# Kernel tuning notes

Hardware: AMD Instinct MI355X
Metric: run time of the kernel (lower is better)

The kernel has to match this reference:

```python
import jax, jax.numpy as jnp
import numpy as np

WD, WH, WW = 1, 7, 7
N = WD * WH * WW  # 49 tokens per window
LN_EPS = 1e-5


def _make_rel_coords_table():
    rd = np.arange(-(WD - 1), WD, dtype=np.float32)
    rh = np.arange(-(WH - 1), WH, dtype=np.float32)
    rw = np.arange(-(WW - 1), WW, dtype=np.float32)
    g = np.stack(np.meshgrid(rd, rh, rw, indexing='ij'), axis=-1)  # (2wd-1,2wh-1,2ww-1,3)
    eps = 1e-6
    g = g / (np.array([WD, WH, WW], np.float32) - (1.0 - eps))
    g = g * 8.0
    g = np.sign(g) * np.log2(np.abs(g) + 1.0) / np.log2(8.0)
    return g[None].astype(np.float32)  # (1,2wd-1,2wh-1,2ww-1,3)


def _make_rel_pos_index():
    coords = np.stack(np.meshgrid(np.arange(WD), np.arange(WH), np.arange(WW), indexing='ij'))
    cf = coords.reshape(3, -1)  # (3,N)
    rel = cf[:, :, None] - cf[:, None, :]  # (3,N,N)
    rel = rel.transpose(1, 2, 0).astype(np.int64)
    rel[..., 0] += WD - 1
    rel[..., 1] += WH - 1
    rel[..., 2] += WW - 1
    rel[..., 0] *= (2 * WH - 1) * (2 * WW - 1)
    rel[..., 1] *= 2 * WW - 1
    return rel.sum(-1).astype(np.int32)  # (N,N)


def setup_inputs() -> dict:
    key = jax.random.key(0)
    ks = jax.random.split(key, 8)
    B, D, H, W, C = 4, 8, 56, 56, 256
    nh, hid = 8, 4 * C

    def init_w(k, shape, fan_in):
        return (jax.random.normal(k, shape, jnp.float32) / np.sqrt(fan_in)).astype(jnp.float32)

    inp = {
        'x': jax.random.normal(ks[0], (B, D, H, W, C), jnp.float32),
        'qkv_w': init_w(ks[1], (3 * C, C), C),
        'q_bias': jnp.zeros((C,), jnp.float32),
        'v_bias': jnp.zeros((C,), jnp.float32),
        'logit_scale': jnp.full((nh, 1, 1), np.log(10.0), jnp.float32),
        'cpb_w1': init_w(ks[2], (512, 3), 3),
        'cpb_b1': jnp.zeros((512,), jnp.float32),
        'cpb_w2': init_w(ks[3], (nh, 512), 512),
        'proj_w': init_w(ks[4], (C, C), C),
        'proj_b': jnp.zeros((C,), jnp.float32),
        'norm1_g': jnp.ones((C,), jnp.float32),
        'norm1_b': jnp.zeros((C,), jnp.float32),
        'fc1_w': init_w(ks[5], (hid, C), C),
        'fc1_b': jnp.zeros((hid,), jnp.float32),
        'fc2_w': init_w(ks[6], (C, hid), hid),
        'fc2_b': jnp.zeros((C,), jnp.float32),
        'norm2_g': jnp.ones((C,), jnp.float32),
        'norm2_b': jnp.zeros((C,), jnp.float32),
        'rel_coords_table': jnp.asarray(_make_rel_coords_table()),
        'rel_pos_index': jnp.asarray(_make_rel_pos_index()),
    }
    return inp


def _layernorm(x, g, b):
    mu = jnp.mean(x, axis=-1, keepdims=True)
    var = jnp.mean(jnp.square(x - mu), axis=-1, keepdims=True)
    return (x - mu) * jax.lax.rsqrt(var + LN_EPS) * g + b


def _l2norm(x):
    # F.normalize(dim=-1): x / max(||x||, 1e-12)
    n = jnp.sqrt(jnp.sum(jnp.square(x), axis=-1, keepdims=True))
    return x / jnp.maximum(n, 1e-12)


def _forward(x, qkv_w, q_bias, v_bias, logit_scale, cpb_w1, cpb_b1, cpb_w2,
             proj_w, proj_b, norm1_g, norm1_b, fc1_w, fc1_b, fc2_w, fc2_b,
             norm2_g, norm2_b, rel_coords_table, rel_pos_index):
    B, D, H, W, C = x.shape
    nh = logit_scale.shape[0]
    hd = C // nh

    # ---- window partition: (B,D,H,W,C) -> (B_, N, C)
    xw = x.reshape(B, D // WD, WD, H // WH, WH, W // WW, WW, C)
    xw = xw.transpose(0, 1, 3, 5, 2, 4, 6, 7).reshape(-1, N, C)
    Bw = xw.shape[0]

    # ---- qkv with (q_bias, 0, v_bias)
    qkv_bias = jnp.concatenate([q_bias, jnp.zeros_like(q_bias), v_bias])
    qkv = xw @ qkv_w.T + qkv_bias  # (Bw,N,3C)
    qkv = qkv.reshape(Bw, N, 3, nh, hd).transpose(2, 0, 3, 1, 4)
    q, k, v = qkv[0], qkv[1], qkv[2]  # (Bw,nh,N,hd)

    # ---- cosine attention with clamped learned logit scale
    attn = jnp.einsum('bhnd,bhmd->bhnm', _l2norm(q), _l2norm(k))
    scale = jnp.exp(jnp.minimum(logit_scale, jnp.float32(np.log(100.0))))  # (nh,1,1)
    attn = attn * scale

    # ---- CPB-MLP relative position bias
    t = rel_coords_table.reshape(-1, 3)
    hcpb = jax.nn.relu(t @ cpb_w1.T + cpb_b1)
    table = hcpb @ cpb_w2.T  # (T, nh)
    rpb = table[rel_pos_index.reshape(-1)].reshape(N, N, nh).transpose(2, 0, 1)
    rpb = 16.0 * jax.nn.sigmoid(rpb)
    attn = attn + rpb[None]

    attn = jax.nn.softmax(attn, axis=-1)
    out = jnp.einsum('bhnm,bhmd->bhnd', attn, v)
    out = out.transpose(0, 2, 1, 3).reshape(Bw, N, C)
    out = out @ proj_w.T + proj_b

    # ---- window reverse
    xr = out.reshape(B, D // WD, H // WH, W // WW, WD, WH, WW, C)
    xr = xr.transpose(0, 1, 4, 2, 5, 3, 6, 7).reshape(B, D, H, W, C)

    # ---- Swin-v2 post-norm residuals
    x = x + _layernorm(xr, norm1_g, norm1_b)
    h = jax.nn.gelu(x @ fc1_w.T + fc1_b, approximate=False)
    y = h @ fc2_w.T + fc2_b
    x = x + _layernorm(y, norm2_g, norm2_b)
    return x


def reference(x, qkv_w, q_bias, v_bias, logit_scale, cpb_w1, cpb_b1, cpb_w2,
              proj_w, proj_b, norm1_g, norm1_b, fc1_w, fc1_b, fc2_w, fc2_b,
              norm2_g, norm2_b, rel_coords_table, rel_pos_index):
    return _forward(x, qkv_w, q_bias, v_bias, logit_scale, cpb_w1, cpb_b1, cpb_w2,
                    proj_w, proj_b, norm1_g, norm1_b, fc1_w, fc1_b, fc2_w, fc2_b,
                    norm2_g, norm2_b, rel_coords_table, rel_pos_index)
```

## Files before the change

### kernel.cpp

```cpp
#include <hip/hip_runtime.h>
#include <hip/hip_bf16.h>

typedef __attribute__((ext_vector_type(8))) short short8_t;
typedef __attribute__((ext_vector_type(4))) float f32x4;

__device__ __forceinline__ float bf2f(unsigned short u) {
    return __uint_as_float(((unsigned)u) << 16);
}
__device__ __forceinline__ unsigned short f2bf(float f) {
    __hip_bfloat16 h = __float2bfloat16(f);
    return *reinterpret_cast<unsigned short*>(&h);
}

__device__ __forceinline__ float fast_gelu(float v) {
    float ax = fabsf(v) * 0.70710678118f;
    float t  = __builtin_amdgcn_rcpf(1.f + 0.3275911f * ax);
    float poly = t * (0.254829592f + t * (-0.284496736f + t * (1.421413741f
               + t * (-1.453152027f + t * 1.061405429f))));
    float e  = __expf(-ax * ax);
    float er = 1.f - poly * e;
    float s  = (v >= 0.f) ? er : -er;
    return 0.5f * v * (1.f + s);
}

__device__ __forceinline__ void async16(const unsigned short* g, unsigned short* l) {
    __builtin_amdgcn_global_load_lds(
        (const __attribute__((address_space(1))) unsigned int*)g,
        (__attribute__((address_space(3))) unsigned int*)l,
        16, 0, 0);
}

__device__ __forceinline__ int win_row_to_token(int r) {
    int wb = r / 49, n = r - wb * 49;
    int wq = wb & 7, hb = (wb >> 3) & 7, d = (wb >> 6) & 7, b = wb >> 9;
    int hh = n / 7, ww2 = n - hh * 7;
    return ((b * 8 + d) * 56 + hb * 7 + hh) * 56 + wq * 7 + ww2;
}

__global__ __launch_bounds__(256) void conv_kernel(
    const float* __restrict__ src, unsigned short* __restrict__ dst, int n4)
{
    int stride = gridDim.x * 256;
    for (int i = blockIdx.x * 256 + threadIdx.x; i < n4; i += stride) {
        float4 v = *reinterpret_cast<const float4*>(&src[(size_t)i * 4]);
        short4 o;
        o.x = (short)f2bf(v.x); o.y = (short)f2bf(v.y);
        o.z = (short)f2bf(v.z); o.w = (short)f2bf(v.w);
        *reinterpret_cast<short4*>(&dst[(size_t)i * 4]) = o;
    }
}

__global__ __launch_bounds__(256) void conv4_kernel(
    const float* __restrict__ s0, unsigned short* __restrict__ d0, int n0,
    const float* __restrict__ s1, unsigned short* __restrict__ d1, int n1,
    const float* __restrict__ s2, unsigned short* __restrict__ d2, int n2,
    const float* __restrict__ s3, unsigned short* __restrict__ d3, int n3)
{
    int stride = gridDim.x * 256;
    int total = n0 + n1 + n2 + n3;
    for (int i = blockIdx.x * 256 + threadIdx.x; i < total; i += stride) {
        const float* s; unsigned short* d; int j = i;
        if (j < n0) { s = s0; d = d0; }
        else if ((j -= n0) < n1) { s = s1; d = d1; }
        else if ((j -= n1) < n2) { s = s2; d = d2; }
        else { j -= n2; s = s3; d = d3; }
        float4 v = *reinterpret_cast<const float4*>(&s[(size_t)j * 4]);
        short4 o;
        o.x = (short)f2bf(v.x); o.y = (short)f2bf(v.y);
        o.z = (short)f2bf(v.z); o.w = (short)f2bf(v.w);
        *reinterpret_cast<short4*>(&d[(size_t)j * 4]) = o;
    }
}

__global__ __launch_bounds__(256) void prep_table_kernel(
    const float* __restrict__ w1, const float* __restrict__ b1,
    const float* __restrict__ w2, const float* __restrict__ tabin,
    float* __restrict__ tableg)
{
    const int i = blockIdx.x;
    const int t = threadIdx.x;
    const float c0 = tabin[i * 3], c1 = tabin[i * 3 + 1], c2 = tabin[i * 3 + 2];
    float part[8] = {0.f, 0.f, 0.f, 0.f, 0.f, 0.f, 0.f, 0.f};
    for (int j = t; j < 512; j += 256) {
        float hv = fmaxf(c0 * w1[j * 3] + c1 * w1[j * 3 + 1] + c2 * w1[j * 3 + 2] + b1[j], 0.f);
        #pragma unroll
        for (int h = 0; h < 8; ++h) part[h] += hv * w2[h * 512 + j];
    }
    #pragma unroll
    for (int h = 0; h < 8; ++h) {
        float v = part[h];
        v += __shfl_xor(v, 1);  v += __shfl_xor(v, 2);  v += __shfl_xor(v, 4);
        v += __shfl_xor(v, 8);  v += __shfl_xor(v, 16); v += __shfl_xor(v, 32);
        part[h] = v;
    }
    __shared__ float red[4][8];
    const int wv = t >> 6, lane = t & 63;
    if (lane == 0) {
        #pragma unroll
        for (int h = 0; h < 8; ++h) red[wv][h] = part[h];
    }
    __syncthreads();
    if (t < 8) tableg[i * 8 + t] = red[0][t] + red[1][t] + red[2][t] + red[3][t];
}

__global__ __launch_bounds__(256) void prep_expand_kernel(
    const float* __restrict__ logit_scale,
    const float* __restrict__ qb, const float* __restrict__ vb,
    const int* __restrict__ rpi, const float* __restrict__ tableg,
    float* __restrict__ scales, float* __restrict__ rpbf,
    float* __restrict__ qkvb)
{
    const int stride = gridDim.x * 256;
    const int gt = blockIdx.x * 256 + threadIdx.x;
    if (gt < 8) scales[gt] = expf(fminf(logit_scale[gt], 4.6051702f));
    for (int i = gt; i < 768; i += stride) {
        float o;
        if (i < 256) o = qb[i];
        else if (i < 512) o = 0.f;
        else o = vb[i - 512];
        qkvb[i] = o;
    }
    for (int e = gt; e < 32768; e += stride) {
        int h = e >> 12, rem = e & 4095;
        int mi = rem >> 10, ji = (rem >> 8) & 3;
        int r16 = (rem >> 4) & 15, g4 = (rem >> 2) & 3, r = rem & 3;
        int i = mi * 16 + g4 * 4 + r, j = ji * 16 + r16;
        float val = 0.f;
        if (i < 49 && j < 49) {
            float xv = tableg[rpi[i * 49 + j] * 8 + h];
            val = 16.f / (1.f + expf(-xv));
        }
        rpbf[e] = val;
    }
}

template<int ACT, int SCATTER>
__global__ __launch_bounds__(256) void gemm_kernel(
    const unsigned short* __restrict__ A, const unsigned short* __restrict__ W,
    const float* __restrict__ bias, unsigned short* __restrict__ C,
    int M, int N, int K, int ntn)
{
    __shared__ unsigned short smem[16384];
    const int tid = threadIdx.x;
    const int lane = tid & 63, wv = tid >> 6;
    const int wr = wv >> 1, wc = wv & 1;
    const int nwg = gridDim.x;
    const int virt = (blockIdx.x & 7) * (nwg >> 3) + (blockIdx.x >> 3);
    const int bn = virt % ntn, bm = virt / ntn;
    const size_t arow0 = (size_t)bm * 128;
    const size_t brow0 = (size_t)bn * 128;
    const int r16 = lane & 15, g4 = lane >> 4;
    const int srow_l = lane >> 2;
    const int sgran  = (lane & 3) ^ ((srow_l >> 1) & 3);
    f32x4 acc[4][4] = {};

    auto STAGE = [&](int buf, int kt) {
        unsigned short* As = smem + buf * 4096;
        unsigned short* Bs = smem + 8192 + buf * 4096;
        #pragma unroll
        for (int i = 0; i < 2; ++i) {
            int row0 = wv * 32 + i * 16;
            async16(&A[(arow0 + row0 + srow_l) * (size_t)K + kt + sgran * 8], &As[row0 * 32]);
            async16(&W[(brow0 + row0 + srow_l) * (size_t)K + kt + sgran * 8], &Bs[row0 * 32]);
        }
    };
    auto COMPUTE = [&](int buf) {
        unsigned short* As = smem + buf * 4096;
        unsigned short* Bs = smem + 8192 + buf * 4096;
        short8_t af[4], bfr[4];
        const int gsw = g4 ^ ((r16 >> 1) & 3);
        #pragma unroll
        for (int m = 0; m < 4; ++m) {
            int row = wr * 64 + m * 16 + r16;
            af[m] = *reinterpret_cast<const short8_t*>(&As[row * 32 + gsw * 8]);
        }
        #pragma unroll
        for (int n = 0; n < 4; ++n) {
            int row = wc * 64 + n * 16 + r16;
            bfr[n] = *reinterpret_cast<const short8_t*>(&Bs[row * 32 + gsw * 8]);
        }
        #pragma unroll
        for (int m = 0; m < 4; ++m)
            #pragma unroll
            for (int n = 0; n < 4; ++n)
                acc[m][n] = __builtin_amdgcn_mfma_f32_16x16x32_bf16(af[m], bfr[n], acc[m][n], 0, 0, 0);
    };

    const int nk = K >> 5;
    STAGE(0, 0);
    STAGE(1, 32);
    int cur = 0;
    for (int ks = 0; ks < nk - 1; ++ks) {
        asm volatile("s_waitcnt vmcnt(4)" ::: "memory");
        __builtin_amdgcn_sched_barrier(0);
        asm volatile("s_barrier" ::: "memory");
        COMPUTE(cur);
        __builtin_amdgcn_sched_barrier(0);
        asm volatile("s_barrier" ::: "memory");
        if (ks + 2 < nk) STAGE(cur, (ks + 2) << 5);
        cur ^= 1;
    }
    asm volatile("s_waitcnt vmcnt(0)" ::: "memory");
    __builtin_amdgcn_sched_barrier(0);
    asm volatile("s_barrier" ::: "memory");
    COMPUTE(cur);
    __builtin_amdgcn_sched_barrier(0);
    asm volatile("s_barrier" ::: "memory");

    unsigned short* Cs = smem + wv * 2432;
    const int rbase = g4 * 4;
    const int srow = lane >> 3, scol = (lane & 7) * 8;
    const int gcol0 = bn * 128 + wc * 64;
    #pragma unroll
    for (int p = 0; p < 2; ++p) {
        #pragma unroll
        for (int n = 0; n < 4; ++n) {
            float bv = bias[bn * 128 + wc * 64 + n * 16 + r16];
            #pragma unroll
            for (int m2 = 0; m2 < 2; ++m2) {
                int m = p * 2 + m2;
                #pragma unroll
                for (int r = 0; r < 4; ++r) {
                    float v = acc[m][n][r] + bv;
                    if (ACT == 1) v = fast_gelu(v);
                    Cs[(m2 * 16 + rbase + r) * 76 + n * 16 + r16] = f2bf(v);
                }
            }
        }
        #pragma unroll
        for (int rr = 0; rr < 4; ++rr) {
            int lr = rr * 8 + srow;
            int grow = bm * 128 + wr * 64 + p * 32 + lr;
            size_t orow = SCATTER ? (size_t)win_row_to_token(grow) : (size_t)grow;
            short8_t vv = *reinterpret_cast<const short8_t*>(&Cs[lr * 76 + scol]);
            *reinterpret_cast<short8_t*>(&C[orow * (size_t)N + gcol0 + scol]) = vv;
        }
    }
}

template<int SCATTER, int OUT_F32>
__global__ __launch_bounds__(512) void gemm_ln_kernel(
    const unsigned short* __restrict__ A, const unsigned short* __restrict__ W,
    const float* __restrict__ bias, const unsigned short* __restrict__ resid,
    const float* __restrict__ gamma, const float* __restrict__ beta,
    void* __restrict__ Cv, int M, int K)
{
    __shared__ unsigned short smem[24576];
    const int tid = threadIdx.x;
    const int lane = tid & 63, wv = tid >> 6;
    const int wr = wv >> 2, wc = wv & 3;
    const int nwg = gridDim.x;
    const int bm = (blockIdx.x & 7) * (nwg >> 3) + (blockIdx.x >> 3);
    const size_t arow0 = (size_t)bm * 128;
    const int r16 = lane & 15, g4 = lane >> 4;
    const int srow_l = lane >> 2;
    const int sgran = (lane & 3) ^ ((srow_l >> 1) & 3);
    f32x4 acc[4][4] = {};

    auto STAGE = [&](int buf, int kt) {
        unsigned short* As = smem + buf * 4096;
        unsigned short* Bs = smem + 8192 + buf * 8192;
        async16(&A[(arow0 + wv * 16 + srow_l) * (size_t)K + kt + sgran * 8],
                &As[(wv * 16) * 32]);
        #pragma unroll
        for (int i = 0; i < 2; ++i) {
            int row0 = wv * 32 + i * 16;
            async16(&W[(size_t)(row0 + srow_l) * K + kt + sgran * 8], &Bs[row0 * 32]);
        }
    };
    auto COMPUTE = [&](int buf) {
        unsigned short* As = smem + buf * 4096;
        unsigned short* Bs = smem + 8192 + buf * 8192;
        short8_t af[4], bfr[4];
        const int gsw = g4 ^ ((r16 >> 1) & 3);
        #pragma unroll
        for (int m = 0; m < 4; ++m) {
            int row = wr * 64 + m * 16 + r16;
            af[m] = *reinterpret_cast<const short8_t*>(&As[row * 32 + gsw * 8]);
        }
        #pragma unroll
        for (int n = 0; n < 4; ++n) {
            int row = wc * 64 + n * 16 + r16;
            bfr[n] = *reinterpret_cast<const short8_t*>(&Bs[row * 32 + gsw * 8]);
        }
        #pragma unroll
        for (int m = 0; m < 4; ++m)
            #pragma unroll
            for (int n = 0; n < 4; ++n)
                acc[m][n] = __builtin_amdgcn_mfma_f32_16x16x32_bf16(af[m], bfr[n], acc[m][n], 0, 0, 0);
    };

    const int nk = K >> 5;
    STAGE(0, 0);
    STAGE(1, 32);
    int cur = 0;
    for (int ks = 0; ks < nk - 1; ++ks) {
        asm volatile("s_waitcnt vmcnt(3)" ::: "memory");
        __builtin_amdgcn_sched_barrier(0);
        asm volatile("s_barrier" ::: "memory");
        COMPUTE(cur);
        __builtin_amdgcn_sched_barrier(0);
        asm volatile("s_barrier" ::: "memory");
        if (ks + 2 < nk) STAGE(cur, (ks + 2) << 5);
        cur ^= 1;
    }
    asm volatile("s_waitcnt vmcnt(0)" ::: "memory");
    __builtin_amdgcn_sched_barrier(0);
    asm volatile("s_barrier" ::: "memory");
    COMPUTE(cur);
    __builtin_amdgcn_sched_barrier(0);
    asm volatile("s_barrier" ::: "memory");

    float bv[4];
    #pragma unroll
    for (int n = 0; n < 4; ++n) bv[n] = bias[wc * 64 + n * 16 + r16];
    float* psum  = reinterpret_cast<float*>(smem + 19456);
    float* psq   = psum + 512;
    float* stats = psq + 512;
    #pragma unroll
    for (int m = 0; m < 4; ++m) {
        #pragma unroll
        for (int r = 0; r < 4; ++r) {
            float s = 0.f, s2 = 0.f;
            #pragma unroll
            for (int n = 0; n < 4; ++n) {
                float v = acc[m][n][r] + bv[n];
                s += v; s2 += v * v;
            }
            s  += __shfl_xor(s, 1);  s  += __shfl_xor(s, 2);
            s  += __shfl_xor(s, 4);  s  += __shfl_xor(s, 8);
            s2 += __shfl_xor(s2, 1); s2 += __shfl_xor(s2, 2);
            s2 += __shfl_xor(s2, 4); s2 += __shfl_xor(s2, 8);
            if (r16 == 0) {
                int row = wr * 64 + m * 16 + g4 * 4 + r;
                psum[row * 4 + wc] = s;
                psq[row * 4 + wc]  = s2;
            }
        }
    }
    __syncthreads();
    if (tid < 128) {
        f32x4 a = *reinterpret_cast<const f32x4*>(&psum[tid * 4]);
        f32x4 b = *reinterpret_cast<const f32x4*>(&psq[tid * 4]);
        float mu  = (a[0] + a[1] + a[2] + a[3]) * 0.00390625f;
        float ex2 = (b[0] + b[1] + b[2] + b[3]) * 0.00390625f;
        stats[tid * 2]     = mu;
        stats[tid * 2 + 1] = rsqrtf(ex2 - mu * mu + 1e-5f);
    }
    __syncthreads();

    unsigned short* Cs = smem + wv * 2432;
    const int rbase = g4 * 4;
    const int srow = lane >> 3, scol = (lane & 7) * 8;
    const int gcol0 = wc * 64;
    f32x4 gm0 = *reinterpret_cast<const f32x4*>(&gamma[gcol0 + scol]);
    f32x4 gm1 = *reinterpret_cast<const f32x4*>(&gamma[gcol0 + scol + 4]);
    f32x4 bt0 = *reinterpret_cast<const f32x4*>(&beta[gcol0 + scol]);
    f32x4 bt1 = *reinterpret_cast<const f32x4*>(&beta[gcol0 + scol + 4]);
    #pragma unroll
    for (int p = 0; p < 2; ++p) {
        #pragma unroll
        for (int n = 0; n < 4; ++n)
            #pragma unroll
            for (int m2 = 0; m2 < 2; ++m2)
                #pragma unroll
                for (int r = 0; r < 4; ++r)
                    Cs[(m2 * 16 + rbase + r) * 76 + n * 16 + r16] =
                        f2bf(acc[p * 2 + m2][n][r] + bv[n]);
        #pragma unroll
        for (int rr = 0; rr < 4; ++rr) {
            int lr = rr * 8 + srow;
            int lrow = wr * 64 + p * 32 + lr;
            int grow = bm * 128 + lrow;
            size_t orow = SCATTER ? (size_t)win_row_to_token(grow) : (size_t)grow;
            float mu  = stats[lrow * 2];
            float inv = stats[lrow * 2 + 1];
            short8_t cv = *reinterpret_cast<const short8_t*>(&Cs[lr * 76 + scol]);
            short8_t rv = *reinterpret_cast<const short8_t*>(&resid[orow * 256 + gcol0 + scol]);
            float o[8];
            #pragma unroll
            for (int e = 0; e < 8; ++e) {
                float g = (e < 4) ? gm0[e] : gm1[e - 4];
                float bb = (e < 4) ? bt0[e] : bt1[e - 4];
                o[e] = bf2f((unsigned short)rv[e])
                     + (bf2f((unsigned short)cv[e]) - mu) * inv * g + bb;
            }
            if (OUT_F32) {
                float* outp = (float*)Cv + orow * 256 + gcol0 + scol;
                f32x4 o0, o1;
                #pragma unroll
                for (int e = 0; e < 4; ++e) { o0[e] = o[e]; o1[e] = o[e + 4]; }
                *reinterpret_cast<f32x4*>(outp)     = o0;
                *reinterpret_cast<f32x4*>(outp + 4) = o1;
            } else {
                unsigned short* outp = (unsigned short*)Cv + orow * 256 + gcol0 + scol;
                short8_t ov;
                #pragma unroll
                for (int e = 0; e < 8; ++e) ov[e] = (short)f2bf(o[e]);
                *reinterpret_cast<short8_t*>(outp) = ov;
            }
        }
    }
}

__global__ __launch_bounds__(64) void attn_kernel(
    const unsigned short* __restrict__ qkv, const float* __restrict__ scales,
    const float* __restrict__ rpbf, unsigned short* __restrict__ out)
{
    constexpr int QO = 0;
    constexpr int KO = 2560;
    constexpr int VO = 5120;
    constexpr int PO = 0;
    __shared__ unsigned short lds[7424];

    const int blk = blockIdx.x;
    const int h = blk & 7, wb = blk >> 3;
    const int lane = threadIdx.x;
    const int r16 = lane & 15, g4 = lane >> 4;

    const int wq = wb & 7, hb = (wb >> 3) & 7, dd = (wb >> 6) & 7, bb2 = wb >> 9;
    const int tok_base = ((bb2 * 8 + dd) * 56 + hb * 7) * 56 + wq * 7;
    const float sc = scales[h];

    {
        short8_t z = {};
        int d = lane >> 1, j0 = 48 + (lane & 1) * 8;
        *reinterpret_cast<short8_t*>(&lds[VO + d * 72 + j0]) = z;
    }
    #pragma unroll
    for (int sel = 0; sel < 2; ++sel) {
        for (int c = lane; c < 196; c += 64) {
            int row = c >> 2, gi = c & 3;
            int tok = tok_base + (row / 7) * 56 + (row % 7);
            const unsigned short* gp = qkv + (size_t)tok * 768 + sel * 256 + h * 32 + gi * 8;
            short8_t raw = *reinterpret_cast<const short8_t*>(gp);
            float f[8]; float ss = 0.f;
            #pragma unroll
            for (int e = 0; e < 8; ++e) { f[e] = bf2f((unsigned short)raw[e]); ss += f[e] * f[e]; }
            ss += __shfl_xor(ss, 1); ss += __shfl_xor(ss, 2);
            float inv = 1.f / fmaxf(sqrtf(ss), 1e-12f);
            if (sel == 0) inv *= sc;
            short8_t o;
            #pragma unroll
            for (int e = 0; e < 8; ++e) o[e] = (short)f2bf(f[e] * inv);
            *reinterpret_cast<short8_t*>(&lds[(sel ? KO : QO) + row * 40 + gi * 8]) = o;
        }
    }
    for (int c = lane; c < 196; c += 64) {
        int j = c >> 2, gi = c & 3;
        int tok = tok_base + (j / 7) * 56 + (j % 7);
        short8_t raw = *reinterpret_cast<const short8_t*>(
            qkv + (size_t)tok * 768 + 512 + h * 32 + gi * 8);
        #pragma unroll
        for (int e = 0; e < 8; ++e)
            lds[VO + (gi * 8 + e) * 72 + j] = (unsigned short)raw[e];
    }
    __syncthreads();

    short8_t qf[4], kf[4];
    #pragma unroll
    for (int mi = 0; mi < 4; ++mi)
        qf[mi] = *reinterpret_cast<const short8_t*>(&lds[QO + (mi * 16 + r16) * 40 + g4 * 8]);
    #pragma unroll
    for (int ji = 0; ji < 4; ++ji)
        kf[ji] = *reinterpret_cast<const short8_t*>(&lds[KO + (ji * 16 + r16) * 40 + g4 * 8]);
    f32x4 acc[4][4] = {};
    #pragma unroll
    for (int mi = 0; mi < 4; ++mi)
        #pragma unroll
        for (int ji = 0; ji < 4; ++ji)
            acc[mi][ji] = __builtin_amdgcn_mfma_f32_16x16x32_bf16(qf[mi], kf[ji], acc[mi][ji], 0, 0, 0);
    __syncthreads();

    const float* rbf = rpbf + h * 4096 + r16 * 16 + g4 * 4;
    f32x4 rbv[4][4];
    #pragma unroll
    for (int mi = 0; mi < 4; ++mi)
        #pragma unroll
        for (int ji = 0; ji < 4; ++ji)
            rbv[mi][ji] = *reinterpret_cast<const f32x4*>(&rbf[(mi * 4 + ji) * 256]);

    #pragma unroll
    for (int mi = 0; mi < 4; ++mi) {
        #pragma unroll
        for (int r = 0; r < 4; ++r) {
            int i = mi * 16 + g4 * 4 + r;
            float s[4]; float m = -1e30f;
            #pragma unroll
            for (int ji = 0; ji < 4; ++ji) {
                int j = ji * 16 + r16;
                float v = acc[mi][ji][r] + rbv[mi][ji][r];
                s[ji] = (j < 49) ? v : -1e30f;
                m = fmaxf(m, s[ji]);
            }
            m = fmaxf(m, __shfl_xor(m, 1)); m = fmaxf(m, __shfl_xor(m, 2));
            m = fmaxf(m, __shfl_xor(m, 4)); m = fmaxf(m, __shfl_xor(m, 8));
            float p[4]; float sum = 0.f;
            #pragma unroll
            for (int ji = 0; ji < 4; ++ji) {
                p[ji] = (s[ji] > -1e29f) ? __expf(s[ji] - m) : 0.f;
                sum += p[ji];
            }
            sum += __shfl_xor(sum, 1); sum += __shfl_xor(sum, 2);
            sum += __shfl_xor(sum, 4); sum += __shfl_xor(sum, 8);
            float rinv = 1.f / sum;
            #pragma unroll
            for (int ji = 0; ji < 4; ++ji) {
                int j = ji * 16 + r16;
                lds[PO + i * 72 + j] = f2bf(p[ji] * rinv);
            }
        }
    }
    __syncthreads();

    f32x4 acc2[4][2] = {};
    #pragma unroll
    for (int ks = 0; ks < 2; ++ks) {
        short8_t pf[4], vf[2];
        int ko = ks * 32 + g4 * 8;
        #pragma unroll
        for (int mi = 0; mi < 4; ++mi)
            pf[mi] = *reinterpret_cast<const short8_t*>(&lds[PO + (mi * 16 + r16) * 72 + ko]);
        #pragma unroll
        for (int ni = 0; ni < 2; ++ni)
            vf[ni] = *reinterpret_cast<const short8_t*>(&lds[VO + (ni * 16 + r16) * 72 + ko]);
        #pragma unroll
        for (int mi = 0; mi < 4; ++mi)
            #pragma unroll
            for (int ni = 0; ni < 2; ++ni)
                acc2[mi][ni] = __builtin_amdgcn_mfma_f32_16x16x32_bf16(pf[mi], vf[ni], acc2[mi][ni], 0, 0, 0);
    }

    #pragma unroll
    for (int mi = 0; mi < 4; ++mi)
        #pragma unroll
        for (int r = 0; r < 4; ++r) {
            int i = mi * 16 + g4 * 4 + r;
            if (i < 49) {
                size_t ob = (size_t)(wb * 49 + i) * 256 + h * 32;
                out[ob + r16]      = f2bf(acc2[mi][0][r]);
                out[ob + 16 + r16] = f2bf(acc2[mi][1][r]);
            }
        }
}

extern "C" void kernel_launch(void* const* d_in, const int* in_sizes, int n_in,
                              void* d_out, int out_size, void* d_ws, size_t ws_size,
                              hipStream_t stream) {
    const float* x      = (const float*)d_in[0];
    const float* qkv_w  = (const float*)d_in[1];
    const float* q_bias = (const float*)d_in[2];
    const float* v_bias = (const float*)d_in[3];
    const float* lscale = (const float*)d_in[4];
    const float* cpb_w1 = (const float*)d_in[5];
    const float* cpb_b1 = (const float*)d_in[6];
    const float* cpb_w2 = (const float*)d_in[7];
    const float* proj_w = (const float*)d_in[8];
    const float* proj_b = (const float*)d_in[9];
    const float* n1g    = (const float*)d_in[10];
    const float* n1b    = (const float*)d_in[11];
    const float* fc1_w  = (const float*)d_in[12];
    const float* fc1_b  = (const float*)d_in[13];
    const float* fc2_w  = (const float*)d_in[14];
    const float* fc2_b  = (const float*)d_in[15];
    const float* n2g    = (const float*)d_in[16];
    const float* n2b    = (const float*)d_in[17];
    const float* rct    = (const float*)d_in[18];
    const int*   rpi    = (const int*)d_in[19];

    char* ws = (char*)d_ws;
    unsigned short* qkv    = (unsigned short*)(ws);
    unsigned short* hbuf   = (unsigned short*)(ws);
    unsigned short* attn_o = (unsigned short*)(ws + 154140672);
    unsigned short* xb     = (unsigned short*)(ws + 205520896);
    unsigned short* x1     = (unsigned short*)(ws + 205520896);
    unsigned short* wqkv   = (unsigned short*)(ws + 308281344);
    unsigned short* wproj  = (unsigned short*)(ws + 308674560);
    unsigned short* wfc1   = (unsigned short*)(ws + 308805632);
    unsigned short* wfc2   = (unsigned short*)(ws + 309329920);
    float*          rpbf   = (float*)(ws + 309854208);
    float*          scales = (float*)(ws + 310378496);
    float*          qkvb   = (float*)(ws + 310378528);
    float*          tableg = (float*)(ws + 310381600);

    const int M = 100352;

    conv_kernel<<<2048, 256, 0, stream>>>(x, xb, 25690112 / 4);
    conv4_kernel<<<768, 256, 0, stream>>>(qkv_w, wqkv, 49152,
                                          proj_w, wproj, 16384,
                                          fc1_w, wfc1, 65536,
                                          fc2_w, wfc2, 65536);
    prep_table_kernel<<<169, 256, 0, stream>>>(cpb_w1, cpb_b1, cpb_w2, rct, tableg);
    prep_expand_kernel<<<128, 256, 0, stream>>>(lscale, q_bias, v_bias, rpi, tableg,
                                                scales, rpbf, qkvb);
    gemm_kernel<0, 0><<<4704, 256, 0, stream>>>(xb, wqkv, qkvb, qkv, M, 768, 256, 6);
    attn_kernel<<<16384, 64, 0, stream>>>(qkv, scales, rpbf, attn_o);
    gemm_ln_kernel<1, 0><<<784, 512, 0, stream>>>(attn_o, wproj, proj_b, xb, n1g, n1b,
                                                  x1, M, 256);
    gemm_kernel<1, 0><<<6272, 256, 0, stream>>>(x1, wfc1, fc1_b, hbuf, M, 1024, 256, 8);
    gemm_ln_kernel<0, 1><<<784, 512, 0, stream>>>(hbuf, wfc2, fc2_b, x1, n2g, n2b,
                                                  d_out, M, 1024);
}
```

Baseline: 465.9 us.

## Fuse fc1, GELU, fc2 and LayerNorm residual into one MLP kernel

Replaces the separate fc1 GEMM (writing a 100352x1024 bf16 hidden buffer) and the fc2 GEMM+LayerNorm kernel with a single kernel. Each 64-row block computes the hidden activations in 256-wide chunks, applies GELU, keeps them in LDS and accumulates fc2 directly, then does the LayerNorm and residual add. This removes the global round trip of the hidden tensor and one launch. In exchange, only 64 rows are processed per block with 4 waves, so weights are re-streamed per block and occupancy is limited by 64KB of LDS.

```diff
diff --git a/kernel.cpp b/kernel.cpp
--- a/kernel.cpp
+++ b/kernel.cpp
@@ -399,6 +399,245 @@
                 for (int e = 0; e < 8; ++e) ov[e] = (short)f2bf(o[e]);
                 *reinterpret_cast<short8_t*>(outp) = ov;
             }
+        }
+    }
+}
+
+__global__ __launch_bounds__(256) void mlp_ln_kernel(
+    const unsigned short* __restrict__ A,
+    const unsigned short* __restrict__ W1,
+    const float* __restrict__ b1,
+    const unsigned short* __restrict__ W2,
+    const float* __restrict__ b2,
+    const float* __restrict__ gamma, const float* __restrict__ beta,
+    float* __restrict__ out, int M)
+{
+    __shared__ unsigned short smem[32768];
+    const int tid = threadIdx.x, lane = tid & 63, wv = tid >> 6;
+    const int wc = wv;
+    const int nwg = gridDim.x;
+    const int bm = (blockIdx.x & 7) * (nwg >> 3) + (blockIdx.x >> 3);
+    const size_t arow0 = (size_t)bm * 64;
+    const int r16 = lane & 15, g4 = lane >> 4;
+    const int srow_l = lane >> 2;
+    const int sgran = (lane & 3) ^ ((srow_l >> 1) & 3);
+    f32x4 accY[4][4] = {};
+
+    auto STAGE_A = [&](int buf, int kt) {
+        int row0 = wv * 16;
+        async16(&A[(arow0 + row0 + srow_l) * 256 + kt + sgran * 8],
+                &smem[buf * 2048 + row0 * 32]);
+    };
+    auto STAGE_W1 = [&](int buf, int c, int kt) {
+        unsigned short* Ws = smem + 16384 + buf * 8192;
+        #pragma unroll
+        for (int i = 0; i < 4; ++i) {
+            int row0 = wv * 64 + i * 16;
+            async16(&W1[(size_t)(c * 256 + row0 + srow_l) * 256 + kt + sgran * 8],
+                    &Ws[row0 * 32]);
+        }
+    };
+    auto STAGE_W2 = [&](int buf, int c, int kt) {
+        unsigned short* Ws = smem + 16384 + buf * 8192;
+        #pragma unroll
+        for (int i = 0; i < 4; ++i) {
+            int row0 = wv * 64 + i * 16;
+            async16(&W2[(size_t)(row0 + srow_l) * 1024 + c * 256 + kt + sgran * 8],
+                    &Ws[row0 * 32]);
+        }
+    };
+
+    for (int c = 0; c < 4; ++c) {
+        f32x4 accT[4][4] = {};
+        STAGE_A(0, 0); STAGE_W1(0, c, 0);
+        __syncthreads();
+        int cur = 0;
+        for (int ks = 1; ks < 8; ++ks) {
+            STAGE_A(cur ^ 1, ks * 32); STAGE_W1(cur ^ 1, c, ks * 32);
+            {
+                unsigned short* As = smem + cur * 2048;
+                unsigned short* Ws = smem + 16384 + cur * 8192;
+                short8_t xf[4], wf[4];
+                const int gsw = g4 ^ ((r16 >> 1) & 3);
+                #pragma unroll
+                for (int mt = 0; mt < 4; ++mt)
+                    xf[mt] = *reinterpret_cast<const short8_t*>(&As[(mt * 16 + r16) * 32 + gsw * 8]);
+                #pragma unroll
+                for (int nt = 0; nt < 4; ++nt)
+                    wf[nt] = *reinterpret_cast<const short8_t*>(&Ws[(wc * 64 + nt * 16 + r16) * 32 + gsw * 8]);
+                #pragma unroll
+                for (int nt = 0; nt < 4; ++nt)
+                    #pragma unroll
+                    for (int mt = 0; mt < 4; ++mt)
+                        accT[nt][mt] = __builtin_amdgcn_mfma_f32_16x16x32_bf16(wf[nt], xf[mt], accT[nt][mt], 0, 0, 0);
+            }
+            __syncthreads();
+            cur ^= 1;
+        }
+        {
+            unsigned short* As = smem + cur * 2048;
+            unsigned short* Ws = smem + 16384 + cur * 8192;
+            short8_t xf[4], wf[4];
+            const int gsw = g4 ^ ((r16 >> 1) & 3);
+            #pragma unroll
+            for (int mt = 0; mt < 4; ++mt)
+                xf[mt] = *reinterpret_cast<const short8_t*>(&As[(mt * 16 + r16) * 32 + gsw * 8]);
+            #pragma unroll
+            for (int nt = 0; nt < 4; ++nt)
+                wf[nt] = *reinterpret_cast<const short8_t*>(&Ws[(wc * 64 + nt * 16 + r16) * 32 + gsw * 8]);
+            #pragma unroll
+            for (int nt = 0; nt < 4; ++nt)
+                #pragma unroll
+                for (int mt = 0; mt < 4; ++mt)
+                    accT[nt][mt] = __builtin_amdgcn_mfma_f32_16x16x32_bf16(wf[nt], xf[mt], accT[nt][mt], 0, 0, 0);
+        }
+        __syncthreads();
+        STAGE_W2(0, c, 0);
+        #pragma unroll
+        for (int nt = 0; nt < 4; ++nt) {
+            f32x4 b1f = *reinterpret_cast<const f32x4*>(&b1[c * 256 + wc * 64 + nt * 16 + g4 * 4]);
+            #pragma unroll
+            for (int mt = 0; mt < 4; ++mt) {
+                int m = mt * 16 + r16;
+                float v0 = fast_gelu(accT[nt][mt][0] + b1f[0]);
+                float v1 = fast_gelu(accT[nt][mt][1] + b1f[1]);
+                float v2 = fast_gelu(accT[nt][mt][2] + b1f[2]);
+                float v3 = fast_gelu(accT[nt][mt][3] + b1f[3]);
+                unsigned lo = ((unsigned)f2bf(v1) << 16) | (unsigned)f2bf(v0);
+                unsigned hi = ((unsigned)f2bf(v3) << 16) | (unsigned)f2bf(v2);
+                int gp = (wc * 8 + nt * 2 + (g4 >> 1)) ^ ((m >> 1) & 7);
+                uint2 val; val.x = lo; val.y = hi;
+                *reinterpret_cast<uint2*>(&smem[m * 256 + gp * 8 + (g4 & 1) * 4]) = val;
+            }
+        }
+        __syncthreads();
+        cur = 0;
+        for (int ks = 1; ks < 8; ++ks) {
+            STAGE_W2(cur ^ 1, c, ks * 32);
+            {
+                unsigned short* Ws = smem + 16384 + cur * 8192;
+                short8_t gf[4], wf2[4];
+                const int kk = ks - 1;
+                #pragma unroll
+                for (int mt = 0; mt < 4; ++mt) {
+                    int m = mt * 16 + r16;
+                    int gp = (kk * 4 + g4) ^ ((m >> 1) & 7);
+                    gf[mt] = *reinterpret_cast<const short8_t*>(&smem[m * 256 + gp * 8]);
+                }
+                const int gsw = g4 ^ ((r16 >> 1) & 3);
+                #pragma unroll
+                for (int nt = 0; nt < 4; ++nt)
+                    wf2[nt] = *reinterpret_cast<const short8_t*>(&Ws[(wc * 64 + nt * 16 + r16) * 32 + gsw * 8]);
+                #pragma unroll
+                for (int mt = 0; mt < 4; ++mt)
+                    #pragma unroll
+                    for (int nt = 0; nt < 4; ++nt)
+                        accY[mt][nt] = __builtin_amdgcn_mfma_f32_16x16x32_bf16(gf[mt], wf2[nt], accY[mt][nt], 0, 0, 0);
+            }
+            __syncthreads();
+            cur ^= 1;
+        }
+        {
+            unsigned short* Ws = smem + 16384 + cur * 8192;
+            short8_t gf[4], wf2[4];
+            #pragma unroll
+            for (int mt = 0; mt < 4; ++mt) {
+                int m = mt * 16 + r16;
+                int gp = (7 * 4 + g4) ^ ((m >> 1) & 7);
+                gf[mt] = *reinterpret_cast<const short8_t*>(&smem[m * 256 + gp * 8]);
+            }
+            const int gsw = g4 ^ ((r16 >> 1) & 3);
+            #pragma unroll
+            for (int nt = 0; nt < 4; ++nt)
+                wf2[nt] = *reinterpret_cast<const short8_t*>(&Ws[(wc * 64 + nt * 16 + r16) * 32 + gsw * 8]);
+            #pragma unroll
+            for (int mt = 0; mt < 4; ++mt)
+                #pragma unroll
+                for (int nt = 0; nt < 4; ++nt)
+                    accY[mt][nt] = __builtin_amdgcn_mfma_f32_16x16x32_bf16(gf[mt], wf2[nt], accY[mt][nt], 0, 0, 0);
+        }
+        __syncthreads();
+    }
+
+    float bv[4];
+    #pragma unroll
+    for (int n = 0; n < 4; ++n) bv[n] = b2[wc * 64 + n * 16 + r16];
+    float* psum  = reinterpret_cast<float*>(smem + 10240);
+    float* psq   = psum + 256;
+    float* stats = psq + 256;
+    #pragma unroll
+    for (int mt = 0; mt < 4; ++mt) {
+        #pragma unroll
+        for (int r = 0; r < 4; ++r) {
+            float s = 0.f, s2 = 0.f;
+            #pragma unroll
+            for (int nt = 0; nt < 4; ++nt) {
+                float v = accY[mt][nt][r] + bv[nt];
+                s += v; s2 += v * v;
+            }
+            s  += __shfl_xor(s, 1);  s  += __shfl_xor(s, 2);
+            s  += __shfl_xor(s, 4);  s  += __shfl_xor(s, 8);
+            s2 += __shfl_xor(s2, 1); s2 += __shfl_xor(s2, 2);
+            s2 += __shfl_xor(s2, 4); s2 += __shfl_xor(s2, 8);
+            if (r16 == 0) {
+                int row = mt * 16 + g4 * 4 + r;
+                psum[row * 4 + wc] = s;
+                psq[row * 4 + wc]  = s2;
+            }
+        }
+    }
+    __syncthreads();
+    if (tid < 64) {
+        f32x4 a = *reinterpret_cast<const f32x4*>(&psum[tid * 4]);
+        f32x4 b = *reinterpret_cast<const f32x4*>(&psq[tid * 4]);
+        float mu  = (a[0] + a[1] + a[2] + a[3]) * 0.00390625f;
+        float ex2 = (b[0] + b[1] + b[2] + b[3]) * 0.00390625f;
+        stats[tid * 2]     = mu;
+        stats[tid * 2 + 1] = rsqrtf(ex2 - mu * mu + 1e-5f);
+    }
+    __syncthreads();
+
+    unsigned short* Cs = smem + wv * 2432;
+    const int rbase = g4 * 4;
+    const int srow = lane >> 3, scol = (lane & 7) * 8;
+    const int gcol0 = wc * 64;
+    f32x4 gm0 = *reinterpret_cast<const f32x4*>(&gamma[gcol0 + scol]);
+    f32x4 gm1 = *reinterpret_cast<const f32x4*>(&gamma[gcol0 + scol + 4]);
+    f32x4 bt0 = *reinterpret_cast<const f32x4*>(&beta[gcol0 + scol]);
+    f32x4 bt1 = *reinterpret_cast<const f32x4*>(&beta[gcol0 + scol + 4]);
+    #pragma unroll
+    for (int p = 0; p < 2; ++p) {
+        #pragma unroll
+        for (int nt = 0; nt < 4; ++nt)
+            #pragma unroll
+            for (int m2 = 0; m2 < 2; ++m2)
+                #pragma unroll
+                for (int r = 0; r < 4; ++r)
+                    Cs[(m2 * 16 + rbase + r) * 76 + nt * 16 + r16] =
+                        f2bf(accY[p * 2 + m2][nt][r] + bv[nt]);
+        #pragma unroll
+        for (int rr = 0; rr < 4; ++rr) {
+            int lr = rr * 8 + srow;
+            int lrow = p * 32 + lr;
+            int grow = bm * 64 + lrow;
+            float mu  = stats[lrow * 2];
+            float inv = stats[lrow * 2 + 1];
+            short8_t cv = *reinterpret_cast<const short8_t*>(&Cs[lr * 76 + scol]);
+            short8_t rv = *reinterpret_cast<const short8_t*>(&A[(size_t)grow * 256 + gcol0 + scol]);
+            float o[8];
+            #pragma unroll
+            for (int e = 0; e < 8; ++e) {
+                float g = (e < 4) ? gm0[e] : gm1[e - 4];
+                float bb = (e < 4) ? bt0[e] : bt1[e - 4];
+                o[e] = bf2f((unsigned short)rv[e])
+                     + (bf2f((unsigned short)cv[e]) - mu) * inv * g + bb;
+            }
+            float* outp = out + (size_t)grow * 256 + gcol0 + scol;
+            f32x4 o0, o1;
+            #pragma unroll
+            for (int e = 0; e < 4; ++e) { o0[e] = o[e]; o1[e] = o[e + 4]; }
+            *reinterpret_cast<f32x4*>(outp)     = o0;
+            *reinterpret_cast<f32x4*>(outp + 4) = o1;
         }
     }
 }
@@ -570,7 +809,6 @@
 
     char* ws = (char*)d_ws;
     unsigned short* qkv    = (unsigned short*)(ws);
-    unsigned short* hbuf   = (unsigned short*)(ws);
     unsigned short* attn_o = (unsigned short*)(ws + 154140672);
     unsigned short* xb     = (unsigned short*)(ws + 205520896);
     unsigned short* x1     = (unsigned short*)(ws + 205520896);
@@ -597,7 +835,6 @@
     attn_kernel<<<16384, 64, 0, stream>>>(qkv, scales, rpbf, attn_o);
     gemm_ln_kernel<1, 0><<<784, 512, 0, stream>>>(attn_o, wproj, proj_b, xb, n1g, n1b,
                                                   x1, M, 256);
-    gemm_kernel<1, 0><<<6272, 256, 0, stream>>>(x1, wfc1, fc1_b, hbuf, M, 1024, 256, 8);
-    gemm_ln_kernel<0, 1><<<784, 512, 0, stream>>>(hbuf, wfc2, fc2_b, x1, n2g, n2b,
-                                                  d_out, M, 1024);
-}
+    mlp_ln_kernel<<<1568, 256, 0, stream>>>(x1, wfc1, fc1_b, wfc2, fc2_b,
+                                            n2g, n2b, (float*)d_out, M);
+}
```

New measurement: 563.3 us. 1.21x slower.
